# Kernel tuning notes

Hardware: AMD Instinct MI355X
Metric: run time of the kernel (lower is better)

## Reference

```python
import jax, jax.numpy as jnp
import numpy as np
from jax import lax

B, FIN, FOUT, K, H, W = 4, 64, 64, 3, 128, 128


def setup_inputs() -> dict:
    key = jax.random.key(0)
    k1, k2, k3, k4, k5 = jax.random.split(key, 5)
    # fan-out per-channel conv weights: one KxK kernel per (out, in) pair
    fan = 1.0 / np.sqrt(K * K)  # torch Conv2d(1,1,K) init scale
    Wf = jax.random.uniform(k1, (FOUT, FIN, K, K), jnp.float32, -fan, fan)
    bf = jax.random.uniform(k2, (FOUT, FIN), jnp.float32, -fan, fan)
    # 1x1 combine: Conv2d(FIN, 1, 1) per output channel
    fc = 1.0 / np.sqrt(FIN)
    Wc = jax.random.uniform(k3, (FOUT, FIN), jnp.float32, -fc, fc)
    bc = jax.random.uniform(k4, (FOUT,), jnp.float32, -fc, fc)
    x = jax.random.normal(k5, (B, FIN, H, W), jnp.float32)
    return {"x": x, "Wf": Wf, "bf": bf, "Wc": Wc, "bc": bc}


def reference(x, Wf, bf, Wc, bc):
    fout, fin, k, _ = Wf.shape
    # Depthwise conv with channel multiplier fout: group i (input channel i)
    # produces output channels i*fout .. i*fout+fout-1, i.e. pair (i, o).
    kern = jnp.transpose(Wf, (2, 3, 1, 0)).reshape(k, k, 1, fin * fout)  # HWIO
    y = lax.conv_general_dilated(
        x, kern, window_strides=(1, 1), padding='VALID',
        dimension_numbers=('NCHW', 'HWIO', 'NCHW'),
        feature_group_count=fin)  # [B, fin*fout, H', W']
    y = y + bf.T.reshape(1, fin * fout, 1, 1)  # bias for pair (i, o)
    y = jax.nn.relu(y)
    b, _, h2, w2 = y.shape
    y = y.reshape(b, fin, fout, h2, w2)
    # 1x1 combine: out[b,o] = sum_i Wc[o,i] * y[b,i,o] + bc[o]
    out = jnp.einsum('biohw,oi->bohw', y, Wc) + bc[None, :, None, None]
    return out
```

## Files before the change

kernel.cpp:

```cpp
#include <hip/hip_runtime.h>

typedef _Float16 f16;
typedef __fp16 h2 __attribute__((ext_vector_type(2)));
typedef f16 f16x4 __attribute__((ext_vector_type(4)));
typedef f16 f16x8 __attribute__((ext_vector_type(8)));
typedef float f32x4 __attribute__((ext_vector_type(4)));
typedef float f32x16 __attribute__((ext_vector_type(16)));
typedef unsigned int uint32;

#define FIN  64
#define FOUT 64
#define HI   128
#define WI   128
#define HO   126
#define WO   126
#define HIWI (HI*WI)
#define NPH  8
#define TR   8
#define TC   16
#define SR   10
#define SDW  12
#define CHSTR (SR*SDW)
#define NSLOT 8
#define ONES_OFF (NSLOT*CHSTR)
#define XBUF (ONES_OFF+SDW)


__global__ __launch_bounds__(256) void prepass(
    const float* __restrict__ Wf, const float* __restrict__ bf,
    const float* __restrict__ Wc, unsigned short* __restrict__ ws)
{
    int t = blockIdx.x * 256 + threadIdx.x;
    if (t < 8192) {
        int i  = t >> 7;
        int ob = (t >> 6) & 1;
        int l  = t & 63;
        int g  = l >> 5, n = l & 31;
        int o  = ob * 32 + n;
        unsigned short h[8];
#pragma unroll
        for (int j = 0; j < 8; ++j) {
            int k = g * 4 + (j & 3) + 8 * (j >> 2);
            float v = 0.0f;
            if (k < 12) {
                int dy = k >> 2, dx = k & 3;
                if (dx < 3) v = Wf[((size_t)o * FIN + i) * 9 + dy * 3 + dx];
            } else if (k == 12) {
                v = bf[o * FIN + i];
            }
            f16 hv = (f16)v;
            h[j] = *(unsigned short*)&hv;
        }
        uint4 pk;
        pk.x = h[0] | ((uint32)h[1] << 16);
        pk.y = h[2] | ((uint32)h[3] << 16);
        pk.z = h[4] | ((uint32)h[5] << 16);
        pk.w = h[6] | ((uint32)h[7] << 16);
        *(uint4*)&ws[(size_t)t * 8] = pk;
    } else if (t < 8192 + 2048) {
        int t2 = t - 8192;
        int ip = t2 >> 6, o = t2 & 63;
        f16 lo = (f16)Wc[(size_t)o * FIN + 2 * ip];
        f16 hi = (f16)Wc[(size_t)o * FIN + 2 * ip + 1];
        uint32 v = (uint32)*(unsigned short*)&lo |
                   ((uint32)*(unsigned short*)&hi << 16);
        ((uint32*)ws)[32768 + t2] = v;
    }
}

__global__ __launch_bounds__(512, 4) void conv_mfma(
    const float* __restrict__ x,  const float* __restrict__ bc,
    const unsigned short* __restrict__ ws, float* __restrict__ out)
{
    __shared__ __align__(16) union {
        struct { uint32 xsl[2][XBUF]; uint32 wcp[32][34]; } a;
        float part[4][64][16];
        float ot[32][132];
    } sm;

    const int tid = threadIdx.x;
    const int l   = tid & 63, w = tid >> 6;
    const int wg  = w >> 2;
    const int wl  = w & 3;
    const int g   = l >> 5;
    const int m   = l & 31;
    const int prow = m >> 2;
    const int qd   = (wl & 1) * 4 + (m & 3);
    const int shl  = (wl >> 1) * 16;
    const int ibase = wg * 32;

    const int fid    = blockIdx.x;
    const int grp    = (fid >> 7) * 8 + (fid & 7);
    const int member = (fid >> 3) & 15;
    const int rx = grp & 15, b = grp >> 4;
    const int cy = member & 7, oh = member >> 3;
    const int row0 = rx * TR;
    const int col0 = cy * TC;
    const int o_lane = oh * 32 + m;

    {
        const uint32* wsrc = ((const uint32*)ws) + 32768;
#pragma unroll
        for (int k = 0; k < 2; ++k) {
            int idx = tid + k * 512;
            int oo = idx >> 5, ip = idx & 31;
            sm.a.wcp[oo][ip] = wsrc[(size_t)ip * 64 + oh * 32 + oo];
        }
    }
    if (tid < 2 * SDW) sm.a.xsl[tid / SDW][ONES_OFF + tid % SDW] = 0x3c003c00u;

    const float* xb = x + (size_t)b * FIN * HIWI;
    const bool stg = (l < 50);
    int goff = 0, widx = 0;
    if (stg) {
        int r = l / 5, u = l % 5;
        int gy = min(row0 + r, HI - 1);
        int gx = min(col0 + 4 * u, WI - 4);
        goff = gy * WI + gx;
        widx = w * CHSTR + r * SDW + 2 * u;
    }
    const int chbase = wg * 32 + wl;

    if (stg) {
        f32x4 v = *(const f32x4*)&xb[(size_t)chbase * HIWI + goff];
        f16x4 h; h[0] = (f16)v[0]; h[1] = (f16)v[1]; h[2] = (f16)v[2]; h[3] = (f16)v[3];
        *(uint2*)&sm.a.xsl[0][widx] = *(uint2*)&h;
    }

    const uint4* Btab = (const uint4*)ws;
    uint4 Bc[4], Bn[4];
#pragma unroll
    for (int c4 = 0; c4 < 4; ++c4)
        Bc[c4] = Btab[(size_t)((ibase + c4) * 2 + oh) * 64 + l];

    f32x16 acc = {}, zero = {};
    const h2 zh = {(__fp16)0.0f, (__fp16)0.0f};

    const int r1off = (prow + g) * SDW + qd;
    const int r2off = g ? (ONES_OFF + qd) : ((prow + 2) * SDW + qd);
    const int r2str = g ? 0 : CHSTR;

    for (int ph = 0; ph < NPH; ++ph) {
        const int cur = ph & 1;
        const bool more = (ph + 1 < NPH);

        f32x4 sv = {};
        if (more) {
            if (stg) sv = *(const f32x4*)
                &xb[(size_t)(chbase + (ph + 1) * 4) * HIWI + goff];
#pragma unroll
            for (int c4 = 0; c4 < 4; ++c4)
                Bn[c4] = Btab[(size_t)((ibase + (ph + 1) * 4 + c4) * 2 + oh) * 64 + l];
        }

        __syncthreads();

        const uint32 wcu0 = sm.a.wcp[m][wg * 16 + ph * 2];
        const uint32 wcu1 = sm.a.wcp[m][wg * 16 + ph * 2 + 1];
        const uint32* base = sm.a.xsl[cur];

#pragma unroll
        for (int c2 = 0; c2 < 2; ++c2) {
            const int ch0 = 2 * c2, ch1 = 2 * c2 + 1;
            const uint32* r1a = base + (wg * 4 + ch0) * CHSTR + r1off;
            const uint32* r2a = base + (wg * 4 + ch0) * r2str + r2off;
            uint32 d0 = r1a[0], d1 = r1a[1], d2 = r1a[2];
            uint32 e0 = r2a[0], e1 = r2a[1], e2 = r2a[2];
            uint4 auv0 = {__builtin_amdgcn_alignbit(d1, d0, shl),
                          __builtin_amdgcn_alignbit(d2, d1, shl),
                          __builtin_amdgcn_alignbit(e1, e0, shl),
                          __builtin_amdgcn_alignbit(e2, e1, shl)};
            f16x8 Af0 = *(f16x8*)&auv0;
            f32x16 S0 = __builtin_amdgcn_mfma_f32_32x32x16_f16(
                            Af0, *(f16x8*)&Bc[ch0], zero, 0, 0, 0);

            const uint32* r1b = base + (wg * 4 + ch1) * CHSTR + r1off;
            const uint32* r2b = base + (wg * 4 + ch1) * r2str + r2off;
            uint32 f0 = r1b[0], f1 = r1b[1], f2 = r1b[2];
            uint32 k0 = r2b[0], k1 = r2b[1], k2 = r2b[2];
            uint4 auv1 = {__builtin_amdgcn_alignbit(f1, f0, shl),
                          __builtin_amdgcn_alignbit(f2, f1, shl),
                          __builtin_amdgcn_alignbit(k1, k0, shl),
                          __builtin_amdgcn_alignbit(k2, k1, shl)};
            f16x8 Af1 = *(f16x8*)&auv1;
            f32x16 S1 = __builtin_amdgcn_mfma_f32_32x32x16_f16(
                            Af1, *(f16x8*)&Bc[ch1], zero, 0, 0, 0);

            const uint32 wcu = c2 ? wcu1 : wcu0;
            h2 wch;
            {
                uint32 t = wcu;
                wch = *(h2*)&t;
            }
#pragma unroll
            for (int r = 0; r < 16; ++r) {
                h2 p = __builtin_amdgcn_cvt_pkrtz(S0[r], S1[r]);
                p = __builtin_elementwise_max(p, zh);
                acc[r] = __builtin_amdgcn_fdot2(p, wch, acc[r], false);
            }
        }

        if (more) {
            if (stg) {
                f16x4 h; h[0] = (f16)sv[0]; h[1] = (f16)sv[1];
                h[2] = (f16)sv[2]; h[3] = (f16)sv[3];
                *(uint2*)&sm.a.xsl[cur ^ 1][widx] = *(uint2*)&h;
            }
#pragma unroll
            for (int c4 = 0; c4 < 4; ++c4) Bc[c4] = Bn[c4];
        }
    }

    __syncthreads();
    if (wg == 1) {
#pragma unroll
        for (int r = 0; r < 16; ++r) sm.part[wl][l][r] = acc[r];
    }
    __syncthreads();
    if (wg == 0) {
#pragma unroll
        for (int r = 0; r < 16; ++r) acc[r] += sm.part[wl][l][r];
    }
    __syncthreads();

    if (wg == 0) {
        const float bcv = bc[o_lane];
#pragma unroll
        for (int r = 0; r < 16; ++r) {
            int p  = (r & 3) + 8 * (r >> 2) + 4 * g;
            int px = (p >> 2) * TC + (wl & 1) * 8 + 2 * (p & 3) + (wl >> 1);
            sm.ot[m][px] = acc[r] + bcv;
        }
    }
    __syncthreads();

    if (tid < 256) {
        const int oo  = tid >> 3;
        const int seg = tid & 7;
        const int o   = oh * 32 + oo;
        const int ho  = row0 + seg;
        if (ho < HO) {
            const float* src = &sm.ot[oo][seg * TC];
            size_t base = ((size_t)(b * FOUT + o) * HO + ho) * WO + col0;
            if (col0 + TC <= WO) {
#pragma unroll
                for (int c = 0; c < TC; ++c) out[base + c] = src[c];
            } else {
#pragma unroll
                for (int c = 0; c < 14; ++c) out[base + c] = src[c];
            }
        }
    }
}

extern "C" void kernel_launch(void* const* d_in, const int* in_sizes, int n_in,
                              void* d_out, int out_size, void* d_ws, size_t ws_size,
                              hipStream_t stream) {
    const float* x  = (const float*)d_in[0];
    const float* Wf = (const float*)d_in[1];
    const float* bf = (const float*)d_in[2];
    const float* Wc = (const float*)d_in[3];
    const float* bc = (const float*)d_in[4];
    float* out = (float*)d_out;
    unsigned short* ws = (unsigned short*)d_ws;

    hipLaunchKernelGGL(prepass, dim3(40), dim3(256), 0, stream, Wf, bf, Wc, ws);

    hipLaunchKernelGGL(conv_mfma, dim3(1024), dim3(512), 0, stream,
                       x, bc, ws, out);
}
```

Measured before the change: 44.54 us.

## Pre-shift and swizzle fp16 input tiles in LDS so MFMA A operands load directly

Input staging now writes each shared-memory row with pre-shifted, overlapping fp16 pairs (36 dwords per row) in an XOR-swizzled column-group order. Each lane can then fetch its MFMA A fragment with two 8-byte LDS reads instead of six scalar reads plus alignbit shifts. The output pixel mapping and the ones row are changed to match the new per-wave column assignment. The cost is three times more LDS data per row, two global loads per staging lane, extra pack conversions, and fewer staging lanes (40 instead of 50).

```diff
diff --git a/kernel.cpp b/kernel.cpp
--- a/kernel.cpp
+++ b/kernel.cpp
@@ -19,11 +19,10 @@
 #define TR   8
 #define TC   16
 #define SR   10
-#define SDW  12
-#define CHSTR (SR*SDW)
-#define NSLOT 8
-#define ONES_OFF (NSLOT*CHSTR)
-#define XBUF (ONES_OFF+SDW)
+#define ROWDW 36
+#define CHSTR (SR*ROWDW)
+#define ONES_DW (8*CHSTR)
+#define XBUF (ONES_DW+2)
 
 
 __global__ __launch_bounds__(256) void prepass(
@@ -85,8 +84,7 @@
     const int g   = l >> 5;
     const int m   = l & 31;
     const int prow = m >> 2;
-    const int qd   = (wl & 1) * 4 + (m & 3);
-    const int shl  = (wl >> 1) * 16;
+    const int wg4 = wg * 4;
     const int ibase = wg * 32;
 
     const int fid    = blockIdx.x;
@@ -107,24 +105,37 @@
             sm.a.wcp[oo][ip] = wsrc[(size_t)ip * 64 + oh * 32 + oo];
         }
     }
-    if (tid < 2 * SDW) sm.a.xsl[tid / SDW][ONES_OFF + tid % SDW] = 0x3c003c00u;
+    if (tid < 4) {
+        int bufi = tid >> 1, d = tid & 1;
+        sm.a.xsl[bufi][ONES_DW + d] = d ? 0u : 0x00003c00u;
+    }
 
     const float* xb = x + (size_t)b * FIN * HIWI;
-    const bool stg = (l < 50);
-    int goff = 0, widx = 0;
+    const bool stg = (l < 40);
+    int goffA = 0, goffB = 0, widx = 0;
     if (stg) {
-        int r = l / 5, u = l % 5;
+        int r = l >> 2, cg = l & 3;
+        int cgsw = cg ^ (r & 3);
         int gy = min(row0 + r, HI - 1);
-        int gx = min(col0 + 4 * u, WI - 4);
-        goff = gy * WI + gx;
-        widx = w * CHSTR + r * SDW + 2 * u;
+        int c0 = col0 + 4 * cg;
+        goffA = gy * WI + min(c0, WI - 4);
+        goffB = gy * WI + min(c0 + 4, WI - 4);
+        widx = w * CHSTR + r * ROWDW + cgsw * 8;
     }
     const int chbase = wg * 32 + wl;
 
     if (stg) {
-        f32x4 v = *(const f32x4*)&xb[(size_t)chbase * HIWI + goff];
-        f16x4 h; h[0] = (f16)v[0]; h[1] = (f16)v[1]; h[2] = (f16)v[2]; h[3] = (f16)v[3];
-        *(uint2*)&sm.a.xsl[0][widx] = *(uint2*)&h;
+        f32x4 vA = *(const f32x4*)&xb[(size_t)chbase * HIWI + goffA];
+        f32x4 vB = *(const f32x4*)&xb[(size_t)chbase * HIWI + goffB];
+        uint32 u0 = __builtin_bit_cast(uint32, __builtin_amdgcn_cvt_pkrtz(vA[0], vA[1]));
+        uint32 u1 = __builtin_bit_cast(uint32, __builtin_amdgcn_cvt_pkrtz(vA[1], vA[2]));
+        uint32 u2 = __builtin_bit_cast(uint32, __builtin_amdgcn_cvt_pkrtz(vA[2], vA[3]));
+        uint32 u3 = __builtin_bit_cast(uint32, __builtin_amdgcn_cvt_pkrtz(vA[3], vB[0]));
+        uint32 u4 = __builtin_bit_cast(uint32, __builtin_amdgcn_cvt_pkrtz(vB[0], vB[1]));
+        uint32 u5 = __builtin_bit_cast(uint32, __builtin_amdgcn_cvt_pkrtz(vB[1], vB[2]));
+        uint32* dst = &sm.a.xsl[0][widx];
+        *(uint4*)(dst + 0) = (uint4){u0, u2, u1, u3};
+        *(uint4*)(dst + 4) = (uint4){u2, u4, u3, u5};
     }
 
     const uint4* Btab = (const uint4*)ws;
@@ -136,18 +147,23 @@
     f32x16 acc = {}, zero = {};
     const h2 zh = {(__fp16)0.0f, (__fp16)0.0f};
 
-    const int r1off = (prow + g) * SDW + qd;
-    const int r2off = g ? (ONES_OFF + qd) : ((prow + 2) * SDW + qd);
+    const int R1  = prow + g;
+    const int r1off = R1 * ROWDW + (4 * (wl ^ (R1 & 3)) + (m & 3)) * 2;
+    const int R2  = prow + 2;
+    const int r2off = g ? ONES_DW : (R2 * ROWDW + (4 * (wl ^ (R2 & 3)) + (m & 3)) * 2);
     const int r2str = g ? 0 : CHSTR;
 
     for (int ph = 0; ph < NPH; ++ph) {
         const int cur = ph & 1;
         const bool more = (ph + 1 < NPH);
 
-        f32x4 sv = {};
+        f32x4 svA = {}, svB = {};
         if (more) {
-            if (stg) sv = *(const f32x4*)
-                &xb[(size_t)(chbase + (ph + 1) * 4) * HIWI + goff];
+            const size_t chn = (size_t)(chbase + (ph + 1) * 4) * HIWI;
+            if (stg) {
+                svA = *(const f32x4*)&xb[chn + goffA];
+                svB = *(const f32x4*)&xb[chn + goffB];
+            }
 #pragma unroll
             for (int c4 = 0; c4 < 4; ++c4)
                 Bn[c4] = Btab[(size_t)((ibase + (ph + 1) * 4 + c4) * 2 + oh) * 64 + l];
@@ -162,26 +178,16 @@
 #pragma unroll
         for (int c2 = 0; c2 < 2; ++c2) {
             const int ch0 = 2 * c2, ch1 = 2 * c2 + 1;
-            const uint32* r1a = base + (wg * 4 + ch0) * CHSTR + r1off;
-            const uint32* r2a = base + (wg * 4 + ch0) * r2str + r2off;
-            uint32 d0 = r1a[0], d1 = r1a[1], d2 = r1a[2];
-            uint32 e0 = r2a[0], e1 = r2a[1], e2 = r2a[2];
-            uint4 auv0 = {__builtin_amdgcn_alignbit(d1, d0, shl),
-                          __builtin_amdgcn_alignbit(d2, d1, shl),
-                          __builtin_amdgcn_alignbit(e1, e0, shl),
-                          __builtin_amdgcn_alignbit(e2, e1, shl)};
+            uint2 A1a = *(const uint2*)(base + (wg4 + ch0) * CHSTR + r1off);
+            uint2 A2a = *(const uint2*)(base + (wg4 + ch0) * r2str + r2off);
+            uint4 auv0 = {A1a.x, A1a.y, A2a.x, A2a.y};
             f16x8 Af0 = *(f16x8*)&auv0;
             f32x16 S0 = __builtin_amdgcn_mfma_f32_32x32x16_f16(
                             Af0, *(f16x8*)&Bc[ch0], zero, 0, 0, 0);
 
-            const uint32* r1b = base + (wg * 4 + ch1) * CHSTR + r1off;
-            const uint32* r2b = base + (wg * 4 + ch1) * r2str + r2off;
-            uint32 f0 = r1b[0], f1 = r1b[1], f2 = r1b[2];
-            uint32 k0 = r2b[0], k1 = r2b[1], k2 = r2b[2];
-            uint4 auv1 = {__builtin_amdgcn_alignbit(f1, f0, shl),
-                          __builtin_amdgcn_alignbit(f2, f1, shl),
-                          __builtin_amdgcn_alignbit(k1, k0, shl),
-                          __builtin_amdgcn_alignbit(k2, k1, shl)};
+            uint2 A1b = *(const uint2*)(base + (wg4 + ch1) * CHSTR + r1off);
+            uint2 A2b = *(const uint2*)(base + (wg4 + ch1) * r2str + r2off);
+            uint4 auv1 = {A1b.x, A1b.y, A2b.x, A2b.y};
             f16x8 Af1 = *(f16x8*)&auv1;
             f32x16 S1 = __builtin_amdgcn_mfma_f32_32x32x16_f16(
                             Af1, *(f16x8*)&Bc[ch1], zero, 0, 0, 0);
@@ -202,9 +208,15 @@
 
         if (more) {
             if (stg) {
-                f16x4 h; h[0] = (f16)sv[0]; h[1] = (f16)sv[1];
-                h[2] = (f16)sv[2]; h[3] = (f16)sv[3];
-                *(uint2*)&sm.a.xsl[cur ^ 1][widx] = *(uint2*)&h;
+                uint32 u0 = __builtin_bit_cast(uint32, __builtin_amdgcn_cvt_pkrtz(svA[0], svA[1]));
+                uint32 u1 = __builtin_bit_cast(uint32, __builtin_amdgcn_cvt_pkrtz(svA[1], svA[2]));
+                uint32 u2 = __builtin_bit_cast(uint32, __builtin_amdgcn_cvt_pkrtz(svA[2], svA[3]));
+                uint32 u3 = __builtin_bit_cast(uint32, __builtin_amdgcn_cvt_pkrtz(svA[3], svB[0]));
+                uint32 u4 = __builtin_bit_cast(uint32, __builtin_amdgcn_cvt_pkrtz(svB[0], svB[1]));
+                uint32 u5 = __builtin_bit_cast(uint32, __builtin_amdgcn_cvt_pkrtz(svB[1], svB[2]));
+                uint32* dst = &sm.a.xsl[cur ^ 1][widx];
+                *(uint4*)(dst + 0) = (uint4){u0, u2, u1, u3};
+                *(uint4*)(dst + 4) = (uint4){u2, u4, u3, u5};
             }
 #pragma unroll
             for (int c4 = 0; c4 < 4; ++c4) Bc[c4] = Bn[c4];
@@ -228,7 +240,7 @@
 #pragma unroll
         for (int r = 0; r < 16; ++r) {
             int p  = (r & 3) + 8 * (r >> 2) + 4 * g;
-            int px = (p >> 2) * TC + (wl & 1) * 8 + 2 * (p & 3) + (wl >> 1);
+            int px = (p >> 2) * TC + wl * 4 + (p & 3);
             sm.ot[m][px] = acc[r] + bcv;
         }
     }
```

Measured after the change: 46.81 us. +5.1%, slower.
